# Kernel optimization log

Hardware: AMD Instinct MI355X
Metric: run time of the kernel (lower is better)

The kernel has to match this reference:

```python
import jax, jax.numpy as jnp
import numpy as np

B, S, D, E, F = 4, 2048, 1024, 8, 4096


def setup_inputs() -> dict:
    key = jax.random.key(0)
    k0, k1, k2, k3 = jax.random.split(key, 4)
    x = jax.random.normal(k0, (B, S, D), dtype=jnp.float32)
    wg = jax.random.normal(k1, (D, E), dtype=jnp.float32) * 0.02       # router
    w_gate = jax.random.normal(k2, (E, D, F), dtype=jnp.float32) * 0.02  # expert gate_proj
    w_down = jax.random.normal(k3, (E, F, D), dtype=jnp.float32) * 0.02  # expert down_proj
    return {"x": x, "wg": wg, "w_gate": w_gate, "w_down": w_down}


def reference(x, wg, w_gate, w_down):
    Bb, Ss, Dd = x.shape
    Ee = wg.shape[1]
    T = Bb * Ss
    C = 2 * T // Ee  # GShard top-2 capacity
    tokens = x.reshape(T, Dd)

    # ---- Top2Gate (fp32 gating) ----
    logits = tokens.astype(jnp.float32) @ wg.astype(jnp.float32)  # [T,E]
    gates = jax.nn.softmax(logits, axis=-1)
    idx1 = jnp.argmax(gates, axis=-1)                              # [T]
    mask1 = jax.nn.one_hot(idx1, Ee, dtype=jnp.int32)
    logits_no1 = jnp.where(mask1 > 0, -jnp.inf, logits)
    idx2 = jnp.argmax(logits_no1, axis=-1)
    mask2 = jax.nn.one_hot(idx2, Ee, dtype=jnp.int32)

    g1 = jnp.take_along_axis(gates, idx1[:, None], axis=-1)[:, 0]
    g2 = jnp.take_along_axis(gates, idx2[:, None], axis=-1)[:, 0]
    denom = jnp.clip(g1 + g2, 1e-9, None)
    g1, g2 = g1 / denom, g2 / denom

    # slot positions: exclusive cumsum per expert; 2nd choice offset by expert's 1st-choice count
    loc1 = jnp.cumsum(mask1, axis=0) - mask1                       # [T,E]
    loc2 = jnp.cumsum(mask2, axis=0) - mask2 + jnp.sum(mask1, axis=0, keepdims=True)
    loc1_s = jnp.sum(loc1 * mask1, axis=-1)                        # [T]
    loc2_s = jnp.sum(loc2 * mask2, axis=-1)
    keep1 = (loc1_s < C).astype(x.dtype)
    keep2 = (loc2_s < C).astype(x.dtype)

    f1 = idx1 * C + jnp.minimum(loc1_s, C - 1)                     # flat [E*C] slot ids
    f2 = idx2 * C + jnp.minimum(loc2_s, C - 1)

    # ---- dispatch (scatter, equivalent to einsum with dispatch_mask) ----
    disp = jnp.zeros((Ee * C, Dd), dtype=x.dtype)
    disp = disp.at[f1].add(tokens * keep1[:, None])
    disp = disp.at[f2].add(tokens * keep2[:, None])
    disp = disp.reshape(Ee, C, Dd)

    # ---- per-expert FFN: down_proj(gelu(gate_proj(x))) ----
    h = jax.nn.gelu(jnp.einsum('ecd,edf->ecf', disp, w_gate), approximate=False)
    eo = jnp.einsum('ecf,efd->ecd', h, w_down).reshape(Ee * C, Dd)

    # ---- combine ----
    out = (g1 * keep1)[:, None].astype(x.dtype) * eo[f1] \
        + (g2 * keep2)[:, None].astype(x.dtype) * eo[f2]
    return out.reshape(Bb, Ss, Dd)
```

## Files before the change

### kernel.cpp

```cpp
#include <hip/hip_runtime.h>
#include <hip/hip_bf16.h>
#include <math.h>

#define TT 8192
#define DDIM 1024
#define EE 8
#define FF 4096
#define CCAP 2048
#define NSLOT 16384

typedef __attribute__((ext_vector_type(4))) float f32x4;
typedef __attribute__((ext_vector_type(8))) short bf16x8;

typedef const __attribute__((address_space(1))) void CGV;
typedef __attribute__((address_space(3))) void LDSV;

__device__ __forceinline__ short f2bf(float f) {
  unsigned u = __builtin_bit_cast(unsigned, f);
  u += 0x7fffu + ((u >> 16) & 1u);
  return (short)(u >> 16);
}
__device__ __forceinline__ float bf2f(short s) {
  unsigned u = ((unsigned)(unsigned short)s) << 16;
  return __builtin_bit_cast(float, u);
}

__global__ void __launch_bounds__(256) gate_kernel(const float* __restrict__ x,
    const float* __restrict__ wg, int* __restrict__ idx1, int* __restrict__ idx2,
    float* __restrict__ g1s, float* __restrict__ g2s) {
  int lane = threadIdx.x & 63;
  int t = blockIdx.x * 4 + (threadIdx.x >> 6);
  const float* xr = x + (size_t)t * DDIM;
  float acc[8];
#pragma unroll
  for (int e = 0; e < 8; ++e) acc[e] = 0.f;
#pragma unroll
  for (int i = 0; i < 4; ++i) {
    int d = lane * 4 + i * 256;
    f32x4 xv = *(const f32x4*)(xr + d);
#pragma unroll
    for (int j = 0; j < 4; ++j) {
      const f32x4* wr = (const f32x4*)(wg + (size_t)(d + j) * 8);
      f32x4 w0 = wr[0], w1 = wr[1];
#pragma unroll
      for (int e = 0; e < 4; ++e) { acc[e] += xv[j] * w0[e]; acc[e + 4] += xv[j] * w1[e]; }
    }
  }
#pragma unroll
  for (int e = 0; e < 8; ++e) {
#pragma unroll
    for (int o = 32; o > 0; o >>= 1) acc[e] += __shfl_xor(acc[e], o, 64);
  }
  if (lane == 0) {
    int i1 = 0; float l1 = acc[0];
#pragma unroll
    for (int e = 1; e < 8; ++e) if (acc[e] > l1) { l1 = acc[e]; i1 = e; }
    int i2 = -1; float l2 = -3.0e38f;
#pragma unroll
    for (int e = 0; e < 8; ++e) if (e != i1 && acc[e] > l2) { l2 = acc[e]; i2 = e; }
    float e2 = expf(l2 - l1);
    float inv = 1.f / (1.f + e2);
    idx1[t] = i1; idx2[t] = i2;
    g1s[t] = inv; g2s[t] = e2 * inv;
  }
}

__global__ void __launch_bounds__(1024) scan_kernel(const int* __restrict__ idx1,
    const int* __restrict__ idx2, const float* __restrict__ g1s, const float* __restrict__ g2s,
    int* __restrict__ f1, int* __restrict__ f2, float* __restrict__ gg1, float* __restrict__ gg2,
    int* __restrict__ slot_token) {
  __shared__ unsigned long long slo[1024], shi[1024];
  int tid = threadIdx.x;
  for (int i = tid; i < NSLOT; i += 1024) slot_token[i] = -1;
  int t0 = tid * 8;
  int e1[8], e2[8];
#pragma unroll
  for (int i = 0; i < 8; ++i) { e1[i] = idx1[t0 + i]; e2[i] = idx2[t0 + i]; }

  unsigned long long lo = 0, hi = 0;
#pragma unroll
  for (int i = 0; i < 8; ++i) {
    int e = e1[i];
    if (e < 4) lo += 1ull << (16 * e); else hi += 1ull << (16 * (e - 4));
  }
  slo[tid] = lo; shi[tid] = hi; __syncthreads();
  for (int off = 1; off < 1024; off <<= 1) {
    unsigned long long alo = 0, ahi = 0;
    if (tid >= off) { alo = slo[tid - off]; ahi = shi[tid - off]; }
    __syncthreads();
    slo[tid] += alo; shi[tid] += ahi;
    __syncthreads();
  }
  unsigned long long exlo = slo[tid] - lo, exhi = shi[tid] - hi;
  unsigned long long tlo = slo[1023], thi = shi[1023];
  __syncthreads();
  int base1[8], tot1[8];
#pragma unroll
  for (int e = 0; e < 4; ++e) {
    base1[e]     = (int)((exlo >> (16 * e)) & 0xFFFF);
    base1[e + 4] = (int)((exhi >> (16 * e)) & 0xFFFF);
    tot1[e]      = (int)((tlo  >> (16 * e)) & 0xFFFF);
    tot1[e + 4]  = (int)((thi  >> (16 * e)) & 0xFFFF);
  }

  lo = 0; hi = 0;
#pragma unroll
  for (int i = 0; i < 8; ++i) {
    int e = e2[i];
    if (e < 4) lo += 1ull << (16 * e); else hi += 1ull << (16 * (e - 4));
  }
  slo[tid] = lo; shi[tid] = hi; __syncthreads();
  for (int off = 1; off < 1024; off <<= 1) {
    unsigned long long alo = 0, ahi = 0;
    if (tid >= off) { alo = slo[tid - off]; ahi = shi[tid - off]; }
    __syncthreads();
    slo[tid] += alo; shi[tid] += ahi;
    __syncthreads();
  }
  exlo = slo[tid] - lo; exhi = shi[tid] - hi;
  int base2[8];
#pragma unroll
  for (int e = 0; e < 4; ++e) {
    base2[e]     = (int)((exlo >> (16 * e)) & 0xFFFF);
    base2[e + 4] = (int)((exhi >> (16 * e)) & 0xFFFF);
  }

#pragma unroll
  for (int i = 0; i < 8; ++i) {
    int t = t0 + i;
    int a = e1[i];
    int p1 = base1[a]++;
    int k1 = (p1 < CCAP);
    int s1 = a * CCAP + (k1 ? p1 : CCAP - 1);
    f1[t] = s1;
    gg1[t] = k1 ? g1s[t] : 0.f;
    if (k1) slot_token[s1] = t;

    int b = e2[i];
    int p2 = base2[b] + tot1[b];
    base2[b]++;
    int k2 = (p2 < CCAP);
    int s2 = b * CCAP + (k2 ? p2 : CCAP - 1);
    f2[t] = s2;
    gg2[t] = k2 ? g2s[t] : 0.f;
    if (k2) slot_token[s2] = t;
  }
}

__global__ void __launch_bounds__(128) dispatch_kernel(const float* __restrict__ x,
    const int* __restrict__ slot_token, short* __restrict__ disp) {
  int slot = blockIdx.x;
  int tid = threadIdx.x;
  int tok = slot_token[slot];
  short* dst = disp + (size_t)slot * DDIM + tid * 8;
  bf16x8 v;
  if (tok >= 0) {
    const float* src = x + (size_t)tok * DDIM + tid * 8;
    f32x4 a = *(const f32x4*)src;
    f32x4 b = *(const f32x4*)(src + 4);
#pragma unroll
    for (int j = 0; j < 4; ++j) { v[j] = f2bf(a[j]); v[j + 4] = f2bf(b[j]); }
  } else {
#pragma unroll
    for (int j = 0; j < 8; ++j) v[j] = 0;
  }
  *(bf16x8*)dst = v;
}

__global__ void __launch_bounds__(256) tconv_kernel(const float* __restrict__ in,
    short* __restrict__ outp, int R, int Cc) {
  __shared__ float tl[32][33];
  long e = blockIdx.z;
  const float* src = in + e * (long)R * Cc;
  short* dst = outp + e * (long)R * Cc;
  int x0 = blockIdx.x * 32, y0 = blockIdx.y * 32;
  int tx = threadIdx.x, ty = threadIdx.y;
#pragma unroll
  for (int r = 0; r < 4; ++r)
    tl[ty * 4 + r][tx] = src[(long)(y0 + ty * 4 + r) * Cc + x0 + tx];
  __syncthreads();
#pragma unroll
  for (int r = 0; r < 4; ++r)
    dst[(long)(x0 + ty * 4 + r) * R + y0 + tx] = f2bf(tl[tx][ty * 4 + r]);
}

template<int KD, int LDA, int LDB, int LDC, bool GELU>
__global__ void __launch_bounds__(256, 4) gemm128(const short* __restrict__ Ag,
    const short* __restrict__ Bg, short* __restrict__ Cg,
    long aes, long bes, long ces, int nbx, int nby) {
  constexpr int KT = KD / 32;
  __shared__ alignas(16) short ldsA[2][128 * 32];
  __shared__ alignas(16) short ldsB[2][128 * 32];

  int bid = blockIdx.x;
  int wid = (bid & 7) * ((int)gridDim.x >> 3) + (bid >> 3);
  int bx = wid % nbx;
  int rem = wid / nbx;
  int by = rem % nby;
  int e  = rem / nby;

  const short* A = Ag + (long)e * aes + (long)by * 128 * LDA;
  const short* B = Bg + (long)e * bes + (long)bx * 128 * LDB;
  short* Cp = Cg + (long)e * ces + (long)by * 128 * LDC + bx * 128;

  int tid = threadIdx.x;
  int l = tid & 63;
  int w = tid >> 6;
  int wm = w >> 1, wn = w & 1;

  f32x4 acc[4][4];
#pragma unroll
  for (int m = 0; m < 4; ++m)
#pragma unroll
    for (int n = 0; n < 4; ++n)
#pragma unroll
      for (int r = 0; r < 4; ++r) acc[m][n][r] = 0.f;

  auto STAGE = [&](int buf, int kt) {
#pragma unroll
    for (int c = 0; c < 2; ++c) {
      int g = c * 256 + tid;
      int row = g >> 2, sl = g & 3;
      int col = kt * 32 + ((sl ^ ((row >> 1) & 3)) << 3);
      __builtin_amdgcn_global_load_lds((CGV*)(A + (long)row * LDA + col),
                                       (LDSV*)(&ldsA[buf][g * 8]), 16, 0, 0);
      __builtin_amdgcn_global_load_lds((CGV*)(B + (long)row * LDB + col),
                                       (LDSV*)(&ldsB[buf][g * 8]), 16, 0, 0);
    }
  };

  int kq = l >> 4;

  STAGE(0, 0);
  __syncthreads();

  for (int t = 0; t < KT; ++t) {
    int cur = t & 1;
    if (t + 1 < KT) STAGE(cur ^ 1, t + 1);

    bf16x8 a[4], b[4];
#pragma unroll
    for (int mm = 0; mm < 4; ++mm) {
      int row = wm * 64 + mm * 16 + (l & 15);
      const char* rp = (const char*)&ldsA[cur][row * 32];
      a[mm] = *(const bf16x8*)(rp + ((kq ^ ((row >> 1) & 3)) << 4));
    }
#pragma unroll
    for (int nn = 0; nn < 4; ++nn) {
      int row = wn * 64 + nn * 16 + (l & 15);
      const char* rp = (const char*)&ldsB[cur][row * 32];
      b[nn] = *(const bf16x8*)(rp + ((kq ^ ((row >> 1) & 3)) << 4));
    }

#pragma unroll
    for (int mm = 0; mm < 4; ++mm)
#pragma unroll
      for (int nn = 0; nn < 4; ++nn)
        acc[mm][nn] = __builtin_amdgcn_mfma_f32_16x16x32_bf16(
            a[mm], b[nn], acc[mm][nn], 0, 0, 0);

    if (t + 1 < KT) __syncthreads();
  }

#pragma unroll
  for (int m = 0; m < 4; ++m) {
    int gr0 = wm * 64 + m * 16 + (l >> 4) * 4;
#pragma unroll
    for (int r = 0; r < 4; ++r) {
#pragma unroll
      for (int n = 0; n < 4; ++n) {
        float vv = acc[m][n][r];
        if (GELU) vv = 0.5f * vv * (1.f + erff(vv * 0.70710678118654752f));
        Cp[(long)(gr0 + r) * LDC + wn * 64 + n * 16 + (l & 15)] = f2bf(vv);
      }
    }
  }
}

__global__ void __launch_bounds__(128) combine_kernel(const short* __restrict__ eo,
    const int* __restrict__ f1, const int* __restrict__ f2,
    const float* __restrict__ gg1, const float* __restrict__ gg2, float* __restrict__ out) {
  int t = blockIdx.x, tid = threadIdx.x;
  float a = gg1[t], b = gg2[t];
  long s1 = f1[t], s2 = f2[t];
  bf16x8 v1 = *(const bf16x8*)(eo + s1 * DDIM + tid * 8);
  bf16x8 v2 = *(const bf16x8*)(eo + s2 * DDIM + tid * 8);
  f32x4 o0, o1;
#pragma unroll
  for (int j = 0; j < 4; ++j) {
    o0[j] = a * bf2f(v1[j])     + b * bf2f(v2[j]);
    o1[j] = a * bf2f(v1[j + 4]) + b * bf2f(v2[j + 4]);
  }
  float* dst = out + (size_t)t * DDIM + tid * 8;
  *(f32x4*)dst = o0;
  *(f32x4*)(dst + 4) = o1;
}

extern "C" void kernel_launch(void* const* d_in, const int* in_sizes, int n_in,
                              void* d_out, int out_size, void* d_ws, size_t ws_size,
                              hipStream_t stream) {
  const float* x      = (const float*)d_in[0];
  const float* wg     = (const float*)d_in[1];
  const float* w_gate = (const float*)d_in[2];
  const float* w_down = (const float*)d_in[3];
  float* out = (float*)d_out;

  char* ws = (char*)d_ws;
  size_t off = 0;
  auto alloc = [&](size_t bytes) -> void* {
    void* p = ws + off;
    off += (bytes + 255) & ~(size_t)255;
    return p;
  };
  short* wbg  = (short*)alloc((size_t)EE * FF * DDIM * 2);
  short* wbd  = (short*)alloc((size_t)EE * DDIM * FF * 2);
  short* disp = (short*)alloc((size_t)NSLOT * DDIM * 2);
  short* eo   = (short*)alloc((size_t)NSLOT * DDIM * 2);
  int*   idx1 = (int*)alloc(TT * 4);
  int*   idx2 = (int*)alloc(TT * 4);
  int*   f1   = (int*)alloc(TT * 4);
  int*   f2   = (int*)alloc(TT * 4);
  float* g1s  = (float*)alloc(TT * 4);
  float* g2s  = (float*)alloc(TT * 4);
  float* gg1  = (float*)alloc(TT * 4);
  float* gg2  = (float*)alloc(TT * 4);
  int*   slot_token = (int*)alloc(NSLOT * 4);
  size_t h_full = (size_t)NSLOT * FF * 2;
  bool full = (off + h_full) <= ws_size;
  short* h = (short*)(ws + off);

  tconv_kernel<<<dim3(FF / 32, DDIM / 32, EE), dim3(32, 8), 0, stream>>>(w_gate, wbg, DDIM, FF);
  tconv_kernel<<<dim3(DDIM / 32, FF / 32, EE), dim3(32, 8), 0, stream>>>(w_down, wbd, FF, DDIM);

  gate_kernel<<<TT / 4, 256, 0, stream>>>(x, wg, idx1, idx2, g1s, g2s);
  scan_kernel<<<1, 1024, 0, stream>>>(idx1, idx2, g1s, g2s, f1, f2, gg1, gg2, slot_token);
  dispatch_kernel<<<NSLOT, 128, 0, stream>>>(x, slot_token, disp);

  if (full) {
    gemm128<DDIM, DDIM, DDIM, FF, true><<<(FF / 128) * (CCAP / 128) * EE, 256, 0, stream>>>(
        disp, wbg, h, (long)CCAP * DDIM, (long)FF * DDIM, (long)CCAP * FF, FF / 128, CCAP / 128);
    gemm128<FF, FF, FF, DDIM, false><<<(DDIM / 128) * (CCAP / 128) * EE, 256, 0, stream>>>(
        h, wbd, eo, (long)CCAP * FF, (long)DDIM * FF, (long)CCAP * DDIM, DDIM / 128, CCAP / 128);
  } else {
    for (int e = 0; e < EE; ++e) {
      gemm128<DDIM, DDIM, DDIM, FF, true><<<(FF / 128) * (CCAP / 128), 256, 0, stream>>>(
          disp + (long)e * CCAP * DDIM, wbg + (long)e * FF * DDIM, h, 0, 0, 0, FF / 128, CCAP / 128);
      gemm128<FF, FF, FF, DDIM, false><<<(DDIM / 128) * (CCAP / 128), 256, 0, stream>>>(
          h, wbd + (long)e * DDIM * FF, eo + (long)e * CCAP * DDIM, 0, 0, 0, DDIM / 128, CCAP / 128);
    }
  }

  combine_kernel<<<TT, 128, 0, stream>>>(eo, f1, f2, gg1, gg2, out);
}
```

Before: 511.0 us.

## Triple-buffer GEMM LDS staging with explicit vmcnt waits

The bf16 expert GEMM goes from a double-buffered to a triple-buffered LDS pipeline. It prefetches two k-tiles ahead and replaces __syncthreads with partial s_waitcnt vmcnt waits plus raw barriers, so global-to-LDS loads have more time in flight. LDS per block grows by half and the launch-bounds occupancy hint drops from 4 to 3 blocks per CU. The hand-counted vmcnt values must match the number of outstanding loads issued per stage.

Result: slower. 589.4 us (+15.4%).

```diff
diff --git a/kernel.cpp b/kernel.cpp
--- a/kernel.cpp
+++ b/kernel.cpp
@@ -14,6 +14,11 @@
 
 typedef const __attribute__((address_space(1))) void CGV;
 typedef __attribute__((address_space(3))) void LDSV;
+
+#define VMC(n)  do { asm volatile("s_waitcnt vmcnt(" #n ")" ::: "memory"); \
+                     __builtin_amdgcn_sched_barrier(0); } while (0)
+#define BAR()   do { __builtin_amdgcn_sched_barrier(0); __builtin_amdgcn_s_barrier(); \
+                     __builtin_amdgcn_sched_barrier(0); } while (0)
 
 __device__ __forceinline__ short f2bf(float f) {
   unsigned u = __builtin_bit_cast(unsigned, f);
@@ -185,12 +190,12 @@
 }
 
 template<int KD, int LDA, int LDB, int LDC, bool GELU>
-__global__ void __launch_bounds__(256, 4) gemm128(const short* __restrict__ Ag,
+__global__ void __launch_bounds__(256, 3) gemm128(const short* __restrict__ Ag,
     const short* __restrict__ Bg, short* __restrict__ Cg,
     long aes, long bes, long ces, int nbx, int nby) {
   constexpr int KT = KD / 32;
-  __shared__ alignas(16) short ldsA[2][128 * 32];
-  __shared__ alignas(16) short ldsB[2][128 * 32];
+  __shared__ alignas(16) short ldsA[3][128 * 32];
+  __shared__ alignas(16) short ldsB[3][128 * 32];
 
   int bid = blockIdx.x;
   int wid = (bid & 7) * ((int)gridDim.x >> 3) + (bid >> 3);
@@ -216,39 +221,42 @@
 #pragma unroll
       for (int r = 0; r < 4; ++r) acc[m][n][r] = 0.f;
 
-  auto STAGE = [&](int buf, int kt) {
+  auto STAGE = [&](int slot, int kt) {
 #pragma unroll
     for (int c = 0; c < 2; ++c) {
       int g = c * 256 + tid;
       int row = g >> 2, sl = g & 3;
       int col = kt * 32 + ((sl ^ ((row >> 1) & 3)) << 3);
       __builtin_amdgcn_global_load_lds((CGV*)(A + (long)row * LDA + col),
-                                       (LDSV*)(&ldsA[buf][g * 8]), 16, 0, 0);
+                                       (LDSV*)(&ldsA[slot][g * 8]), 16, 0, 0);
       __builtin_amdgcn_global_load_lds((CGV*)(B + (long)row * LDB + col),
-                                       (LDSV*)(&ldsB[buf][g * 8]), 16, 0, 0);
+                                       (LDSV*)(&ldsB[slot][g * 8]), 16, 0, 0);
     }
   };
 
   int kq = l >> 4;
 
   STAGE(0, 0);
-  __syncthreads();
-
+  STAGE(1, 1);
+  VMC(4);
+  BAR();
+
+  int sl0 = 0;
   for (int t = 0; t < KT; ++t) {
-    int cur = t & 1;
-    if (t + 1 < KT) STAGE(cur ^ 1, t + 1);
+    int sl2 = sl0 + 2; if (sl2 >= 3) sl2 -= 3;
+    if (t + 2 < KT) STAGE(sl2, t + 2);
 
     bf16x8 a[4], b[4];
 #pragma unroll
     for (int mm = 0; mm < 4; ++mm) {
       int row = wm * 64 + mm * 16 + (l & 15);
-      const char* rp = (const char*)&ldsA[cur][row * 32];
+      const char* rp = (const char*)&ldsA[sl0][row * 32];
       a[mm] = *(const bf16x8*)(rp + ((kq ^ ((row >> 1) & 3)) << 4));
     }
 #pragma unroll
     for (int nn = 0; nn < 4; ++nn) {
       int row = wn * 64 + nn * 16 + (l & 15);
-      const char* rp = (const char*)&ldsB[cur][row * 32];
+      const char* rp = (const char*)&ldsB[sl0][row * 32];
       b[nn] = *(const bf16x8*)(rp + ((kq ^ ((row >> 1) & 3)) << 4));
     }
 
@@ -259,7 +267,12 @@
         acc[mm][nn] = __builtin_amdgcn_mfma_f32_16x16x32_bf16(
             a[mm], b[nn], acc[mm][nn], 0, 0, 0);
 
-    if (t + 1 < KT) __syncthreads();
+    if (t + 1 < KT) {
+      if (t + 2 < KT) { VMC(4); }
+      else            { VMC(0); }
+      BAR();
+    }
+    sl0 = (sl0 == 2) ? 0 : sl0 + 1;
   }
 
 #pragma unroll
```
